# Kernel optimization log

Measured on AMD Instinct MI355X. Metric: run time of the kernel, lower is better.

## Reference

```python
import jax, jax.numpy as jnp
import numpy as np

H = 1024
L = 2

def setup_inputs() -> dict:
    key = jax.random.key(0)
    k1, k2, k3, k4, k5 = jax.random.split(key, 5)
    B, S = 32, 2048
    scale = 1.0 / np.sqrt(H)
    return {
        "query": jax.random.normal(k1, (B, 1, H * L), dtype=jnp.float32),
        "keys": jax.random.normal(k2, (B, S, H), dtype=jnp.float32),
        "Wa_w": jax.random.normal(k3, (H * L, H), dtype=jnp.float32) * scale,
        "Wa_b": jnp.zeros((H,), dtype=jnp.float32),
        "Ua_w": jax.random.normal(k4, (H, H), dtype=jnp.float32) * scale,
        "Ua_b": jnp.zeros((H,), dtype=jnp.float32),
        "Va_w": jax.random.normal(k5, (H, 1), dtype=jnp.float32) * scale,
        "Va_b": jnp.zeros((1,), dtype=jnp.float32),
    }

def reference(query, keys, Wa_w, Wa_b, Ua_w, Ua_b, Va_w, Va_b):
    # query: [B,1,H*L], keys: [B,S,H]
    q = jnp.einsum('bqd,dh->bqh', query, Wa_w) + Wa_b   # [B,1,H]
    k = jnp.einsum('bsd,dh->bsh', keys, Ua_w) + Ua_b    # [B,S,H]
    e = jnp.tanh(q + k)                                  # [B,S,H]
    scores = jnp.einsum('bsh,ho->bso', e, Va_w) + Va_b   # [B,S,1]
    scores = scores[:, :, 0][:, None, :]                 # [B,1,S]
    weights = jax.nn.softmax(scores, axis=-1)            # [B,1,S]
    context = jnp.einsum('bqs,bsh->bqh', weights, keys)  # [B,1,H]
    return (context, weights)
```

## Files before the change

### kernel.cpp

```cpp
#include <hip/hip_runtime.h>
#include <hip/hip_bf16.h>


typedef __attribute__((ext_vector_type(8))) short short8;
typedef __attribute__((ext_vector_type(4))) float floatx4;

typedef const __attribute__((address_space(1))) unsigned int gu32;
typedef __attribute__((address_space(3))) unsigned int lu32;

__device__ __forceinline__ unsigned short f2bf(float f) {
    union { float f; unsigned int u; } c; c.f = f;
    unsigned int u = c.u + 0x7fffu + ((c.u >> 16) & 1u);
    return (unsigned short)(u >> 16);
}

__device__ __forceinline__ unsigned int f2bf2(float lo, float hi) {
#if __has_builtin(__builtin_amdgcn_cvt_pk_bf16_f32)
    auto r = __builtin_amdgcn_cvt_pk_bf16_f32(lo, hi);
    unsigned int u; __builtin_memcpy(&u, &r, 4);
    return u;
#else
    return (unsigned int)f2bf(lo) | ((unsigned int)f2bf(hi) << 16);
#endif
}

__device__ __forceinline__ void gld16(const unsigned short* g, unsigned short* l) {
    __builtin_amdgcn_global_load_lds(
        (gu32*)(uintptr_t)g,
        (lu32*)(unsigned int)(uintptr_t)l,
        16, 0, 0);
}

__device__ __forceinline__ void kb16_chunk(const float* __restrict__ keys,
                                           unsigned short* __restrict__ kb,
                                           unsigned int t)
{
    unsigned int rg  = t >> 7;
    unsigned int rem = t & 127u;
    unsigned int g   = rem >> 2;
    unsigned int c   = rem & 3u;
    unsigned int p   = ((rg & 2047u) >> 1) & 3u;
    const float4* src = reinterpret_cast<const float4*>(keys + (size_t)rg*1024 + g*32 + c*8);
    float4 v0 = src[0], v1 = src[1];
    uint4 w;
    w.x = f2bf2(v0.x, v0.y); w.y = f2bf2(v0.z, v0.w);
    w.z = f2bf2(v1.x, v1.y); w.w = f2bf2(v1.z, v1.w);
    *reinterpret_cast<uint4*>(kb + (size_t)rg*1024 + g*32 + ((c ^ p) << 3)) = w;
}

__global__ __launch_bounds__(256) void pre_k(
    const float* __restrict__ query, const float* __restrict__ Wa,
    const float* __restrict__ Wab, const float* __restrict__ Uab,
    const float* __restrict__ Ua, const float* __restrict__ keys,
    float* __restrict__ qws, unsigned short* __restrict__ uat,
    unsigned short* __restrict__ kb, unsigned int kb_nch)
{
    __shared__ char smem[12288];
    const int tid = threadIdx.x;
    if (blockIdx.x < 512) {
        float* qs  = (float*)smem;
        float* red = (float*)(smem + 8192);
        const int b = blockIdx.x >> 4, hc = blockIdx.x & 15;
        #pragma unroll
        for (int i = 0; i < 8; i++) qs[tid + 256*i] = query[b*2048 + tid + 256*i];
        __syncthreads();
        const int hq = tid & 15;
        const int dg = tid >> 4;
        const float4* wp = reinterpret_cast<const float4*>(Wa + (size_t)(dg*128)*1024 + hc*64 + hq*4);
        const float* qp = qs + dg*128;
        float4 a0; a0.x = a0.y = a0.z = a0.w = 0.f;
        float4 a1; a1.x = a1.y = a1.z = a1.w = 0.f;
        #pragma unroll 4
        for (int d = 0; d < 128; d += 2) {
            float q0 = qp[d], q1 = qp[d+1];
            float4 w0 = wp[(size_t)d*256];
            float4 w1 = wp[(size_t)(d+1)*256];
            a0.x += q0*w0.x; a0.y += q0*w0.y; a0.z += q0*w0.z; a0.w += q0*w0.w;
            a1.x += q1*w1.x; a1.y += q1*w1.y; a1.z += q1*w1.z; a1.w += q1*w1.w;
        }
        a0.x += a1.x; a0.y += a1.y; a0.z += a1.z; a0.w += a1.w;
        *reinterpret_cast<float4*>(red + dg*64 + hq*4) = a0;
        __syncthreads();
        if (tid < 64) {
            float v = 0.f;
            #pragma unroll
            for (int g = 0; g < 16; g++) v += red[g*64 + tid];
            int hh = hc*64 + tid;
            qws[b*1024 + hh] = v + Wab[hh] + Uab[hh];
        }
    } else if (blockIdx.x < 768) {
        typedef unsigned short row_t[65];
        row_t* t = (row_t*)smem;
        const int q = blockIdx.x - 512;
        const int x = tid & 63, yy = tid >> 6;
        const int d0 = (q >> 4)*64, h0 = (q & 15)*64;
        #pragma unroll
        for (int i = 0; i < 16; i++) {
            int y = yy*16 + i;
            t[y][x] = f2bf(Ua[(size_t)(d0+y)*1024 + h0 + x]);
        }
        __syncthreads();
        #pragma unroll
        for (int i = 0; i < 16; i++) {
            int y = yy*16 + i;
            uat[(size_t)(h0+y)*1024 + d0 + x] = t[x][y];
        }
    } else {
        const unsigned int stride = (gridDim.x - 768u) * 256u;
        unsigned int t = (blockIdx.x - 768u)*256u + tid;
        #pragma unroll 4
        for (int it = 0; it < 4; ++it, t += stride)
            if (t < kb_nch) kb16_chunk(keys, kb, t);
    }
}

__global__ __launch_bounds__(256) void kb16_k(const float* __restrict__ keys,
                                              unsigned short* __restrict__ kb,
                                              unsigned int nch)
{
    const unsigned int stride = gridDim.x * 256u;
    unsigned int t = blockIdx.x * 256u + threadIdx.x;
    #pragma unroll 4
    for (int it = 0; it < 4; ++it, t += stride)
        if (t < nch) kb16_chunk(keys, kb, t);
}

__global__ __launch_bounds__(256) void score_gemm_fast(
    const unsigned short* __restrict__ kb16,
    const unsigned short* __restrict__ uat,
    const float* __restrict__ qws,
    const float* __restrict__ Va,
    float* __restrict__ score,
    int b0)
{
    __shared__ unsigned short aS[2][128*32];
    __shared__ unsigned short bS[2][256*32];
    const int tid = threadIdx.x;
    const int bz = blockIdx.z;
    const int b = b0 + bz;
    const int s0 = blockIdx.x * 128;
    const int h0 = blockIdx.y * 256;
    const int lane = tid & 63, wave = tid >> 6;
    const int quad = lane >> 4, l15 = lane & 15;
    const int wm = (wave & 1) * 64, wn = (wave >> 1) * 128;

    const int srow = lane >> 2;
    const int schunk = (lane & 3) ^ ((srow >> 1) & 3);
    const unsigned short* ubase = uat + (size_t)h0*1024;
    size_t boff[4];
    #pragma unroll
    for (int u = 0; u < 4; u++) {
        int cg = wave*4 + u;
        boff[u] = (size_t)(cg*16 + srow)*1024 + schunk*8;
    }

    const unsigned short* kA = kb16 + (size_t)(bz*2048 + s0)*1024;
    const size_t aoff0 = (size_t)(tid >> 2)*1024 + (size_t)(tid & 3)*8;
    const size_t aoff1 = (size_t)(64 + (tid >> 2))*1024 + (size_t)(tid & 3)*8;

    floatx4 acc[4][8];
    #pragma unroll
    for (int i = 0; i < 4; i++)
        #pragma unroll
        for (int j = 0; j < 8; j++) acc[i][j] = (floatx4)0.0f;

    gld16(kA + aoff0, aS[0] + wave*512);
    gld16(kA + aoff1, aS[0] + 2048 + wave*512);
    #pragma unroll
    for (int u = 0; u < 4; u++)
        gld16(ubase + boff[u], bS[0] + (wave*4 + u)*512);
    __syncthreads();

    int cur = 0;
    for (int kt = 0; kt < 31; ++kt) {
        const int nxt = cur ^ 1;
        const int k1 = (kt + 1) << 5;

        gld16(kA + aoff0 + k1, aS[nxt] + wave*512);
        gld16(kA + aoff1 + k1, aS[nxt] + 2048 + wave*512);
        #pragma unroll
        for (int u = 0; u < 4; u++)
            gld16(ubase + boff[u] + k1, bS[nxt] + (wave*4 + u)*512);

        short8 af[4], bf8[8];
        #pragma unroll
        for (int i = 0; i < 4; i++) {
            int row = wm + 16*i + l15;
            af[i] = *reinterpret_cast<const short8*>(aS[cur] + row*32 + ((quad ^ ((row>>1)&3)) * 8));
        }
        #pragma unroll
        for (int j = 0; j < 8; j++) {
            int row = wn + 16*j + l15;
            bf8[j] = *reinterpret_cast<const short8*>(bS[cur] + row*32 + ((quad ^ ((row>>1)&3)) * 8));
        }
        #pragma unroll
        for (int i = 0; i < 4; i++)
            #pragma unroll
            for (int j = 0; j < 8; j++)
                acc[i][j] = __builtin_amdgcn_mfma_f32_16x16x32_bf16(af[i], bf8[j], acc[i][j], 0, 0, 0);

        __syncthreads();
        cur = nxt;
    }

    {
        short8 af[4], bf8[8];
        #pragma unroll
        for (int i = 0; i < 4; i++) {
            int row = wm + 16*i + l15;
            af[i] = *reinterpret_cast<const short8*>(aS[cur] + row*32 + ((quad ^ ((row>>1)&3)) * 8));
        }
        #pragma unroll
        for (int j = 0; j < 8; j++) {
            int row = wn + 16*j + l15;
            bf8[j] = *reinterpret_cast<const short8*>(bS[cur] + row*32 + ((quad ^ ((row>>1)&3)) * 8));
        }
        #pragma unroll
        for (int i = 0; i < 4; i++)
            #pragma unroll
            for (int j = 0; j < 8; j++)
                acc[i][j] = __builtin_amdgcn_mfma_f32_16x16x32_bf16(af[i], bf8[j], acc[i][j], 0, 0, 0);
    }

    float qv[8], vav[8];
    #pragma unroll
    for (int j = 0; j < 8; j++) {
        int n = h0 + wn + 16*j + l15;
        qv[j]  = qws[b*1024 + n];
        vav[j] = Va[n];
    }
    #pragma unroll
    for (int i = 0; i < 4; i++) {
        #pragma unroll
        for (int r = 0; r < 4; r++) {
            float p = 0.f;
            #pragma unroll
            for (int j = 0; j < 8; j++) {
                float x = qv[j] + acc[i][j][r];
                float e = __expf(2.f * x);
                float t = 1.f - 2.f * __builtin_amdgcn_rcpf(e + 1.f);
                p += vav[j] * t;
            }
            #pragma unroll
            for (int off = 1; off < 16; off <<= 1) p += __shfl_xor(p, off, 64);
            if (l15 == 0) {
                int m = wm + 16*i + quad*4 + r;
                atomicAdd(score + (size_t)b*2048 + s0 + m, p);
            }
        }
    }
}

__global__ __launch_bounds__(256) void softmax_k(const float* __restrict__ score,
                                                 float* __restrict__ out_w)
{
    const int tid = threadIdx.x;
    const int b = blockIdx.x;
    __shared__ float wred[4], wred2[4];
    float sc[8];
    float mx = -3.0e38f;
    #pragma unroll
    for (int i = 0; i < 8; i++) {
        sc[i] = score[(size_t)b*2048 + tid + 256*i];
        mx = fmaxf(mx, sc[i]);
    }
    #pragma unroll
    for (int off = 32; off >= 1; off >>= 1) mx = fmaxf(mx, __shfl_xor(mx, off, 64));
    if ((tid & 63) == 0) wred[tid >> 6] = mx;
    __syncthreads();
    mx = fmaxf(fmaxf(wred[0], wred[1]), fmaxf(wred[2], wred[3]));
    float e[8]; float lsum = 0.f;
    #pragma unroll
    for (int i = 0; i < 8; i++) { e[i] = __expf(sc[i] - mx); lsum += e[i]; }
    #pragma unroll
    for (int off = 32; off >= 1; off >>= 1) lsum += __shfl_xor(lsum, off, 64);
    if ((tid & 63) == 0) wred2[tid >> 6] = lsum;
    __syncthreads();
    float inv = 1.0f / (wred2[0] + wred2[1] + wred2[2] + wred2[3]);
    #pragma unroll
    for (int i = 0; i < 8; i++) out_w[b*2048 + tid + 256*i] = e[i] * inv;
}

__global__ __launch_bounds__(256) void ctx_k(const float* __restrict__ keys,
                                             const float* __restrict__ w,
                                             float* __restrict__ out_ctx, int sper)
{
    const int tid = threadIdx.x;
    const int b = blockIdx.x, sc = blockIdx.y;
    const float4* k4 = reinterpret_cast<const float4*>(keys) + (size_t)(b*2048 + sc*sper)*256;
    const float* wp = w + b*2048 + sc*sper;
    float4 a; a.x = a.y = a.z = a.w = 0.f;
    #pragma unroll 4
    for (int s = 0; s < sper; s++) {
        float wv = wp[s];
        float4 kv = k4[(size_t)s*256 + tid];
        a.x += wv*kv.x; a.y += wv*kv.y; a.z += wv*kv.z; a.w += wv*kv.w;
    }
    float* o = out_ctx + (size_t)b*1024 + tid*4;
    atomicAdd(o + 0, a.x);
    atomicAdd(o + 1, a.y);
    atomicAdd(o + 2, a.z);
    atomicAdd(o + 3, a.w);
}

extern "C" void kernel_launch(void* const* d_in, const int* in_sizes, int n_in,
                              void* d_out, int out_size, void* d_ws, size_t ws_size,
                              hipStream_t stream)
{
    const float* query = (const float*)d_in[0];
    const float* keys  = (const float*)d_in[1];
    const float* Wa_w  = (const float*)d_in[2];
    const float* Wa_b  = (const float*)d_in[3];
    const float* Ua_w  = (const float*)d_in[4];
    const float* Ua_b  = (const float*)d_in[5];
    const float* Va_w  = (const float*)d_in[6];

    char* ws = (char*)d_ws;
    float*          qws   = (float*)(ws);
    unsigned short* uat   = (unsigned short*)(ws + 131072);
    float*          score = (float*)(ws + 131072 + 2097152);
    const size_t BASE = 131072 + 2097152 + 4194304 + 2097152;
    unsigned short* kb16 = (unsigned short*)(ws + BASE);

    size_t avail = (ws_size > BASE) ? (ws_size - BASE) : 0;
    int nb = 32;
    while (nb > 1 && (size_t)nb * 2048 * 1024 * 2 > avail) nb >>= 1;

    float* out_ctx = (float*)d_out;
    float* out_w   = out_ctx + 32*1024;

    hipMemsetAsync(score, 0, 32*2048*sizeof(float), stream);
    hipMemsetAsync(out_ctx, 0, 32*1024*sizeof(float), stream);

    if (nb == 32) {
        const unsigned int nch = 32u * 2048u * 128u;
        pre_k<<<dim3(768 + 8192), 256, 0, stream>>>(
            query, Wa_w, Wa_b, Ua_b, Ua_w, keys, qws, uat, kb16, nch);
        score_gemm_fast<<<dim3(16, 4, 32), 256, 0, stream>>>(kb16, uat, qws, Va_w, score, 0);
    } else {
        pre_k<<<dim3(768), 256, 0, stream>>>(
            query, Wa_w, Wa_b, Ua_b, Ua_w, keys, qws, uat, kb16, 0u);
        for (int b0 = 0; b0 < 32; b0 += nb) {
            unsigned int nch = (unsigned int)nb * 2048u * 128u;
            unsigned int nblk = (nch/4u + 255u) / 256u;
            kb16_k<<<dim3(nblk), 256, 0, stream>>>(keys + (size_t)b0*2048*1024, kb16, nch);
            score_gemm_fast<<<dim3(16, 4, nb), 256, 0, stream>>>(kb16, uat, qws, Va_w, score, b0);
        }
    }
    softmax_k<<<dim3(32),     256, 0, stream>>>(score, out_w);
    ctx_k    <<<dim3(32, 16), 256, 0, stream>>>(keys, out_w, out_ctx, 128);
}
```

Measured before the change: 619.6 us.

## Fold memsets into pre kernel and fuse softmax with context reduction

Zeroing of the score and context buffers moves into extra blocks of the preprocessing kernel, which removes two memset launches. Softmax and the context weighted sum are fused into one kernel. Each of 32x64 blocks recomputes the row max and sum over all 2048 scores, then normalizes its own 32 weights and accumulates them against keys. This removes one launch and raises context parallelism, at the cost of redundant softmax reductions and more atomics on the output.

```diff
diff --git a/kernel.cpp b/kernel.cpp
--- a/kernel.cpp
+++ b/kernel.cpp
@@ -53,7 +53,8 @@
     const float* __restrict__ Wab, const float* __restrict__ Uab,
     const float* __restrict__ Ua, const float* __restrict__ keys,
     float* __restrict__ qws, unsigned short* __restrict__ uat,
-    unsigned short* __restrict__ kb, unsigned int kb_nch)
+    unsigned short* __restrict__ kb, unsigned int kb_nch,
+    float* __restrict__ score, float* __restrict__ out_ctx)
 {
     __shared__ char smem[12288];
     const int tid = threadIdx.x;
@@ -105,9 +106,15 @@
             int y = yy*16 + i;
             uat[(size_t)(h0+y)*1024 + d0 + x] = t[x][y];
         }
+    } else if (blockIdx.x < 800) {
+        float* p = score + (size_t)(blockIdx.x - 768) * 2048;
+        for (int i = tid; i < 2048; i += 256) p[i] = 0.f;
+    } else if (blockIdx.x < 832) {
+        float* p = out_ctx + (size_t)(blockIdx.x - 800) * 1024;
+        for (int i = tid; i < 1024; i += 256) p[i] = 0.f;
     } else {
-        const unsigned int stride = (gridDim.x - 768u) * 256u;
-        unsigned int t = (blockIdx.x - 768u)*256u + tid;
+        const unsigned int stride = (gridDim.x - 832u) * 256u;
+        unsigned int t = (blockIdx.x - 832u)*256u + tid;
         #pragma unroll 4
         for (int it = 0; it < 4; ++it, t += stride)
             if (t < kb_nch) kb16_chunk(keys, kb, t);
@@ -251,50 +258,48 @@
     }
 }
 
-__global__ __launch_bounds__(256) void softmax_k(const float* __restrict__ score,
-                                                 float* __restrict__ out_w)
+__global__ __launch_bounds__(256) void ctxsm_k(const float* __restrict__ keys,
+                                               const float* __restrict__ score,
+                                               float* __restrict__ out_w,
+                                               float* __restrict__ out_ctx)
 {
     const int tid = threadIdx.x;
-    const int b = blockIdx.x;
-    __shared__ float wred[4], wred2[4];
-    float sc[8];
+    const int b = blockIdx.x, sc = blockIdx.y;
+    __shared__ float wred[4], wred2[4], wv[32];
+    float sv[8];
     float mx = -3.0e38f;
     #pragma unroll
     for (int i = 0; i < 8; i++) {
-        sc[i] = score[(size_t)b*2048 + tid + 256*i];
-        mx = fmaxf(mx, sc[i]);
+        sv[i] = score[(size_t)b*2048 + tid + 256*i];
+        mx = fmaxf(mx, sv[i]);
     }
     #pragma unroll
     for (int off = 32; off >= 1; off >>= 1) mx = fmaxf(mx, __shfl_xor(mx, off, 64));
     if ((tid & 63) == 0) wred[tid >> 6] = mx;
     __syncthreads();
     mx = fmaxf(fmaxf(wred[0], wred[1]), fmaxf(wred[2], wred[3]));
-    float e[8]; float lsum = 0.f;
-    #pragma unroll
-    for (int i = 0; i < 8; i++) { e[i] = __expf(sc[i] - mx); lsum += e[i]; }
+    float lsum = 0.f;
+    #pragma unroll
+    for (int i = 0; i < 8; i++) lsum += __expf(sv[i] - mx);
     #pragma unroll
     for (int off = 32; off >= 1; off >>= 1) lsum += __shfl_xor(lsum, off, 64);
     if ((tid & 63) == 0) wred2[tid >> 6] = lsum;
     __syncthreads();
-    float inv = 1.0f / (wred2[0] + wred2[1] + wred2[2] + wred2[3]);
-    #pragma unroll
-    for (int i = 0; i < 8; i++) out_w[b*2048 + tid + 256*i] = e[i] * inv;
-}
-
-__global__ __launch_bounds__(256) void ctx_k(const float* __restrict__ keys,
-                                             const float* __restrict__ w,
-                                             float* __restrict__ out_ctx, int sper)
-{
-    const int tid = threadIdx.x;
-    const int b = blockIdx.x, sc = blockIdx.y;
-    const float4* k4 = reinterpret_cast<const float4*>(keys) + (size_t)(b*2048 + sc*sper)*256;
-    const float* wp = w + b*2048 + sc*sper;
+    const float inv = 1.0f / (wred2[0] + wred2[1] + wred2[2] + wred2[3]);
+    if (tid < 32) {
+        float e = __expf(score[(size_t)b*2048 + sc*32 + tid] - mx) * inv;
+        wv[tid] = e;
+        out_w[b*2048 + sc*32 + tid] = e;
+    }
+    __syncthreads();
+
+    const float4* k4 = reinterpret_cast<const float4*>(keys) + (size_t)(b*2048 + sc*32)*256 + tid;
     float4 a; a.x = a.y = a.z = a.w = 0.f;
     #pragma unroll 4
-    for (int s = 0; s < sper; s++) {
-        float wv = wp[s];
-        float4 kv = k4[(size_t)s*256 + tid];
-        a.x += wv*kv.x; a.y += wv*kv.y; a.z += wv*kv.z; a.w += wv*kv.w;
+    for (int s = 0; s < 32; s++) {
+        float w = wv[s];
+        float4 kv = k4[(size_t)s*256];
+        a.x += w*kv.x; a.y += w*kv.y; a.z += w*kv.z; a.w += w*kv.w;
     }
     float* o = out_ctx + (size_t)b*1024 + tid*4;
     atomicAdd(o + 0, a.x);
@@ -329,17 +334,16 @@
     float* out_ctx = (float*)d_out;
     float* out_w   = out_ctx + 32*1024;
 
-    hipMemsetAsync(score, 0, 32*2048*sizeof(float), stream);
-    hipMemsetAsync(out_ctx, 0, 32*1024*sizeof(float), stream);
-
     if (nb == 32) {
         const unsigned int nch = 32u * 2048u * 128u;
-        pre_k<<<dim3(768 + 8192), 256, 0, stream>>>(
-            query, Wa_w, Wa_b, Ua_b, Ua_w, keys, qws, uat, kb16, nch);
+        pre_k<<<dim3(832 + 8192), 256, 0, stream>>>(
+            query, Wa_w, Wa_b, Ua_b, Ua_w, keys, qws, uat, kb16, nch,
+            score, out_ctx);
         score_gemm_fast<<<dim3(16, 4, 32), 256, 0, stream>>>(kb16, uat, qws, Va_w, score, 0);
     } else {
-        pre_k<<<dim3(768), 256, 0, stream>>>(
-            query, Wa_w, Wa_b, Ua_b, Ua_w, keys, qws, uat, kb16, 0u);
+        pre_k<<<dim3(832), 256, 0, stream>>>(
+            query, Wa_w, Wa_b, Ua_b, Ua_w, keys, qws, uat, kb16, 0u,
+            score, out_ctx);
         for (int b0 = 0; b0 < 32; b0 += nb) {
             unsigned int nch = (unsigned int)nb * 2048u * 128u;
             unsigned int nblk = (nch/4u + 255u) / 256u;
@@ -347,6 +351,5 @@
             score_gemm_fast<<<dim3(16, 4, nb), 256, 0, stream>>>(kb16, uat, qws, Va_w, score, b0);
         }
     }
-    softmax_k<<<dim3(32),     256, 0, stream>>>(score, out_w);
-    ctx_k    <<<dim3(32, 16), 256, 0, stream>>>(keys, out_w, out_ctx, 128);
-}
+    ctxsm_k<<<dim3(32, 64), 256, 0, stream>>>(keys, score, out_w, out_ctx);
+}
```

Result: no change. 617.4 us (-0.4%).
